# Optimization experiments

Hardware: AMD Instinct MI355X
Metric: run time of the kernel (lower is better)

Reference implementation:

```python
import jax, jax.numpy as jnp
import numpy as np

LENGTH = 100
EMBED = 64
BATCH = 8192


def setup_inputs() -> dict:
    key = jax.random.key(0)
    k1, k2 = jax.random.split(key)
    x = jax.random.normal(k1, (BATCH, LENGTH), dtype=jnp.float32)
    # learned embedding table (nn.Embedding weight)
    W = jax.random.normal(k2, (LENGTH, EMBED), dtype=jnp.float32)
    return {"x": x, "W": W}


def reference(x, W):
    # Torch module computes: result[b, 0, i*E + j] = x[b, i] * W[i, j]
    # (the sparse selector matmul `x @ trans` merely repeats each x column E times,
    #  and the tiled embedding lookup flattens W per batch row).
    B, L = x.shape
    E = W.shape[1]
    out = x[:, :, None] * W[None, :, :]          # [B, L, E]
    return out.reshape(B, 1, L * E)
```

## Files before the change

kernel.cpp:

```cpp
#include <hip/hip_runtime.h>
#include <hip/hip_bf16.h>


#define LENGTH 100
#define EMBED 64
#define BATCH 8192
#define V4_PER_ROW (LENGTH * EMBED / 4)
#define TPB 320
#define BSLICES 256

typedef float vfloat4 __attribute__((ext_vector_type(4)));

__global__ __launch_bounds__(TPB) void chemical_embedding_kernel(
    const float* __restrict__ x,
    const float* __restrict__ W,
    float* __restrict__ out)
{
    const int r = blockIdx.x * TPB + threadIdx.x;
    const int i = r >> 4;

    const vfloat4 w = reinterpret_cast<const vfloat4*>(W)[r];

    const int b0 = blockIdx.y;
    const float* __restrict__ xp = x + b0 * LENGTH + i;
    vfloat4* __restrict__ op =
        reinterpret_cast<vfloat4*>(out) + (size_t)b0 * V4_PER_ROW + r;

    const int xstep = BSLICES * LENGTH;
    const int ostep = BSLICES * V4_PER_ROW;

#pragma unroll 4
    for (int it = 0; it < BATCH / BSLICES; ++it) {
        const float s = *xp;
        *op = s * w;
        xp += xstep;
        op += ostep;
    }
}

extern "C" void kernel_launch(void* const* d_in, const int* in_sizes, int n_in,
                              void* d_out, int out_size, void* d_ws, size_t ws_size,
                              hipStream_t stream) {
    const float* x = (const float*)d_in[0];
    const float* W = (const float*)d_in[1];
    float* out = (float*)d_out;

    dim3 grid(V4_PER_ROW / TPB, BSLICES);
    chemical_embedding_kernel<<<grid, TPB, 0, stream>>>(x, W, out);
}
```

Before: 206.0 us.

## Use flat grid-stride loop with nontemporal stores for embedding output

```diff
diff --git a/kernel.cpp b/kernel.cpp
--- a/kernel.cpp
+++ b/kernel.cpp
@@ -5,9 +5,11 @@
 #define LENGTH 100
 #define EMBED 64
 #define BATCH 8192
-#define V4_PER_ROW (LENGTH * EMBED / 4)
-#define TPB 320
-#define BSLICES 256
+#define NV4 (BATCH * LENGTH * EMBED / 4)
+#define TPB 256
+#define NBLK 2048
+#define GSTRIDE (TPB * NBLK)
+#define ITERS (NV4 / GSTRIDE)
 
 typedef float vfloat4 __attribute__((ext_vector_type(4)));
 
@@ -16,25 +18,18 @@
     const float* __restrict__ W,
     float* __restrict__ out)
 {
-    const int r = blockIdx.x * TPB + threadIdx.x;
-    const int i = r >> 4;
+    unsigned g = blockIdx.x * TPB + threadIdx.x;
+    const vfloat4* __restrict__ Wv = reinterpret_cast<const vfloat4*>(W);
+    vfloat4* __restrict__ ov = reinterpret_cast<vfloat4*>(out);
 
-    const vfloat4 w = reinterpret_cast<const vfloat4*>(W)[r];
-
-    const int b0 = blockIdx.y;
-    const float* __restrict__ xp = x + b0 * LENGTH + i;
-    vfloat4* __restrict__ op =
-        reinterpret_cast<vfloat4*>(out) + (size_t)b0 * V4_PER_ROW + r;
-
-    const int xstep = BSLICES * LENGTH;
-    const int ostep = BSLICES * V4_PER_ROW;
-
-#pragma unroll 4
-    for (int it = 0; it < BATCH / BSLICES; ++it) {
-        const float s = *xp;
-        *op = s * w;
-        xp += xstep;
-        op += ostep;
+#pragma unroll 5
+    for (int it = 0; it < ITERS; ++it) {
+        const unsigned row = g / 1600u;
+        const unsigned col = g - row * 1600u;
+        const float s = x[row * 100u + (col >> 4)];
+        const vfloat4 v = s * Wv[col];
+        __builtin_nontemporal_store(v, ov + g);
+        g += GSTRIDE;
     }
 }
 
@@ -45,6 +40,5 @@
     const float* W = (const float*)d_in[1];
     float* out = (float*)d_out;
 
-    dim3 grid(V4_PER_ROW / TPB, BSLICES);
-    chemical_embedding_kernel<<<grid, TPB, 0, stream>>>(x, W, out);
+    chemical_embedding_kernel<<<dim3(NBLK), dim3(TPB), 0, stream>>>(x, W, out);
 }
```

Result: slower. 230.9 us (+12.1%).
